# Kernel optimization log

Hardware: AMD Instinct MI355X
Metric: run time of the kernel (lower is better)

## Reference

```python
import jax, jax.numpy as jnp
import numpy as np

N_HEADS = 16
SEG_LEN = 512
MSG_LEN = 1536
T_TOTAL = SEG_LEN + MSG_LEN  # 2048


def _build_mask(T):
    # rows < SEG_LEN: attend to all cols < SEG_LEN (full, non-causal block)
    # rows >= SEG_LEN: standard causal (cols <= row)
    rows = jnp.arange(T)[:, None]
    cols = jnp.arange(T)[None, :]
    mask = jnp.where(rows < SEG_LEN, cols < SEG_LEN, cols <= rows)
    return mask  # [T, T] bool


def setup_inputs() -> dict:
    key = jax.random.key(0)
    k1, k2, k3 = jax.random.split(key, 3)
    B, T, E = 4, T_TOTAL, 1024
    x = jax.random.normal(k1, (B, T, E), dtype=jnp.float32)
    W_qkv = jax.random.normal(k2, (E, 3 * E), dtype=jnp.float32) * (1.0 / np.sqrt(E))
    b_qkv = jnp.zeros((3 * E,), dtype=jnp.float32)
    W_proj = jax.random.normal(k3, (E, E), dtype=jnp.float32) * (1.0 / np.sqrt(E))
    b_proj = jnp.zeros((E,), dtype=jnp.float32)
    return {"x": x, "W_qkv": W_qkv, "b_qkv": b_qkv, "W_proj": W_proj, "b_proj": b_proj}


def reference(x, W_qkv, b_qkv, W_proj, b_proj):
    B, T, E = x.shape
    H = N_HEADS
    D = E // H
    qkv = x @ W_qkv + b_qkv  # [B, T, 3E]
    q, k, v = jnp.split(qkv, 3, axis=-1)
    # [B, H, T, D]
    q = q.reshape(B, T, H, D).transpose(0, 2, 1, 3)
    k = k.reshape(B, T, H, D).transpose(0, 2, 1, 3)
    v = v.reshape(B, T, H, D).transpose(0, 2, 1, 3)
    att = jnp.einsum("bhqd,bhkd->bhqk", q, k) * (1.0 / np.sqrt(D))
    mask = _build_mask(T)  # [T, T]
    att = jnp.where(mask[None, None], att, jnp.float32(-jnp.inf))
    att = jax.nn.softmax(att, axis=-1)
    y = jnp.einsum("bhqk,bhkd->bhqd", att, v)
    y = y.transpose(0, 2, 1, 3).reshape(B, T, E)
    return y @ W_proj + b_proj
```

## Files before the change

### kernel.cpp

```cpp
#include <hip/hip_runtime.h>


typedef _Float16 f16;
typedef _Float16 f16x4 __attribute__((ext_vector_type(4)));
typedef _Float16 f16x8 __attribute__((ext_vector_type(8)));
typedef float f32x4 __attribute__((ext_vector_type(4)));

#define MFMA16x32(a, b, c) __builtin_amdgcn_mfma_f32_16x16x32_f16(a, b, c, 0, 0, 0)
#define MFMA16x16(a, b, c) __builtin_amdgcn_mfma_f32_16x16x16f16(a, b, c, 0, 0, 0)

__device__ __forceinline__ void gload_lds16(const void* g, void* l) {
  __builtin_amdgcn_global_load_lds(
      (__attribute__((address_space(1))) void*)g,
      (__attribute__((address_space(3))) void*)l, 16, 0, 0);
}


__global__ __launch_bounds__(256) void k_prep(
    const float* __restrict__ x, f16* __restrict__ xh,
    const float* __restrict__ Wq, f16* __restrict__ Wqt,
    const float* __restrict__ Wp, f16* __restrict__ Wpt) {
  __shared__ float tile[32][33];
  const int bid = blockIdx.x;
  if (bid < 8192) {
    int i = bid * 256 + threadIdx.x;
    float4 v = ((const float4*)x)[i];
    f16x4 o = {(f16)v.x, (f16)v.y, (f16)v.z, (f16)v.w};
    ((f16x4*)xh)[i] = o;
    return;
  }
  const float* W;
  f16* Wt;
  int Ndim, bx, by;
  if (bid < 8192 + 3072) {
    int r = bid - 8192;
    W = Wq; Wt = Wqt; Ndim = 3072; bx = r % 96; by = r / 96;
  } else {
    int r = bid - 11264;
    W = Wp; Wt = Wpt; Ndim = 1024; bx = r % 32; by = r / 32;
  }
  const int tx = threadIdx.x & 31, ty = threadIdx.x >> 5;
  const int n = bx * 32 + tx;
  const int k0 = by * 32;
  for (int j = ty; j < 32; j += 8)
    tile[j][tx] = W[(size_t)(k0 + j) * Ndim + n];
  __syncthreads();
  const int k = k0 + tx;
  for (int j = ty; j < 32; j += 8)
    Wt[(size_t)(bx * 32 + j) * 1024 + k] = (f16)tile[tx][j];
}


__global__ __launch_bounds__(256) void k_gemm_qkv(
    const f16* __restrict__ A, const f16* __restrict__ Bt,
    const float* __restrict__ bias,
    f16* __restrict__ Qo, f16* __restrict__ Ko, f16* __restrict__ Vo) {
  constexpr int KD = 1024;
  __shared__ __align__(16) f16 smem[2 * 128 * 64];
  f16* As = smem;
  f16* Bs = smem + 128 * 64;
  const int tid = threadIdx.x;
  const int wave = tid >> 6, lane = tid & 63;
  const int g = lane >> 4, l16 = lane & 15;
  const int m0 = blockIdx.y * 128, n0 = blockIdx.x * 128;
  const int wm = (wave >> 1) * 64, wn = (wave & 1) * 64;
  const int srow = wave * 8 + (lane >> 3);
  const int skc = ((lane & 7) ^ (lane >> 3)) * 8;

  f32x4 acc[4][4] = {};

  for (int k0 = 0; k0 < KD; k0 += 64) {
    __syncthreads();
    for (int it = 0; it < 4; ++it) {
      gload_lds16(A + (size_t)(m0 + it * 32 + srow) * KD + k0 + skc,
                  As + (it * 32 + wave * 8) * 64);
      gload_lds16(Bt + (size_t)(n0 + it * 32 + srow) * KD + k0 + skc,
                  Bs + (it * 32 + wave * 8) * 64);
    }
    __syncthreads();
    for (int kk = 0; kk < 64; kk += 32) {
      const int ks = kk >> 3;
      f16x8 af[4], bf[4];
      for (int mi = 0; mi < 4; ++mi) {
        int R = wm + mi * 16 + l16, sw = R & 7;
        af[mi] = *(const f16x8*)(As + R * 64 + ((ks + g) ^ sw) * 8);
      }
      for (int ni = 0; ni < 4; ++ni) {
        int R = wn + ni * 16 + l16, sw = R & 7;
        bf[ni] = *(const f16x8*)(Bs + R * 64 + ((ks + g) ^ sw) * 8);
      }
      for (int mi = 0; mi < 4; ++mi)
        for (int ni = 0; ni < 4; ++ni)
          acc[mi][ni] = MFMA16x32(af[mi], bf[ni], acc[mi][ni]);
    }
  }

  const int nsub = n0 + wn;
  const int part = nsub >> 10;
  const int h    = (nsub >> 6) & 15;
  const int mg   = m0 + wm;
  const int b    = mg >> 11;
  const int tb   = mg & 2047;
  const size_t bh = (size_t)(b * 16 + h);

  float bv[4];
  for (int ni = 0; ni < 4; ++ni) bv[ni] = bias[nsub + ni * 16 + l16];

  __syncthreads();
  f16* Es = smem + wave * 4096;

  for (int mi = 0; mi < 4; ++mi)
    for (int ni = 0; ni < 4; ++ni)
      for (int r = 0; r < 4; ++r) {
        f16 hv = (f16)(acc[mi][ni][r] + bv[ni]);
        int mrow = mi * 16 + g * 4 + r, ncol = ni * 16 + l16;
        if (part == 2)
          Es[ncol * 64 + (mrow ^ ((ncol & 7) << 3))] = hv;
        else
          Es[mrow * 64 + (ncol ^ ((mrow & 7) << 3))] = hv;
      }

  const int rrow = lane >> 3, rj = lane & 7;
  for (int p = 0; p < 8; ++p) {
    int row = p * 8 + rrow;
    f16x8 vv = *(const f16x8*)(Es + row * 64 + (rj ^ (row & 7)) * 8);
    int rcol = rj * 8;
    if (part == 0)
      *(f16x8*)(Qo + (bh * 2048 + tb + row) * 64 + rcol) = vv;
    else if (part == 1)
      *(f16x8*)(Ko + (bh * 2048 + tb + row) * 64 + rcol) = vv;
    else
      *(f16x8*)(Vo + (bh * 64 + row) * 2048 + tb + rcol) = vv;
  }
}


__global__ __launch_bounds__(256, 4) void k_attn(
    const f16* __restrict__ Q, const f16* __restrict__ Kb,
    const f16* __restrict__ Vt, f16* __restrict__ Y) {
  __shared__ __align__(16) f16 Ks[2][64 * 64];
  __shared__ __align__(16) f16 Vs[2][64 * 64];
  __shared__ float rs[4 * 32];

  const int tid = threadIdx.x;
  const int wave = tid >> 6, lane = tid & 63;
  const int g = lane >> 4, l16 = lane & 15;
  const int bh = blockIdx.x;
  const int b = bh >> 4, h = bh & 15;
  const int qt = 15 - blockIdx.y;
  const int q0 = qt * 128;
  const int nt = (qt < 4) ? 8 : (qt + 1) * 2;
  const int srowrel = lane >> 3;
  const int sc = (lane & 7) ^ srowrel;

  const f32x4 sinit = {-8.65617025f, -8.65617025f, -8.65617025f, -8.65617025f};

  f16x8 aq[2][2];
  for (int mi = 0; mi < 2; ++mi) {
    const f16* qrow =
        Q + ((size_t)bh * 2048 + q0 + wave * 32 + mi * 16 + l16) * 64 + g * 8;
    aq[mi][0] = *(const f16x8*)(qrow);
    aq[mi][1] = *(const f16x8*)(qrow + 32);
    for (int kb = 0; kb < 2; ++kb)
      aq[mi][kb] = aq[mi][kb] * (f16)0.18033688f;
  }

  f32x4 o[2][4] = {};
  float rsum[2] = {};

  for (int it = 0; it < 2; ++it) {
    int row = it * 32 + wave * 8 + srowrel;
    gload_lds16(Kb + ((size_t)bh * 2048 + row) * 64 + sc * 8,
                &Ks[0][(it * 32 + wave * 8) * 64]);
    gload_lds16(Vt + ((size_t)bh * 64 + row) * 2048 + sc * 8,
                &Vs[0][(it * 32 + wave * 8) * 64]);
  }
  __syncthreads();

  int cur = 0;
  for (int i = 0; i < nt; ++i) {
    if (i + 1 < nt) {
      const int kn0 = (i + 1) << 6;
      for (int it = 0; it < 2; ++it) {
        int row = it * 32 + wave * 8 + srowrel;
        gload_lds16(Kb + ((size_t)bh * 2048 + kn0 + row) * 64 + sc * 8,
                    &Ks[cur ^ 1][(it * 32 + wave * 8) * 64]);
        gload_lds16(Vt + ((size_t)bh * 64 + row) * 2048 + kn0 + sc * 8,
                    &Vs[cur ^ 1][(it * 32 + wave * 8) * 64]);
      }
    }

    const int kt0 = i << 6;
    const f16* Kc = Ks[cur];
    const f16* Vc = Vs[cur];

    f32x4 t[2][4];
    for (int nb = 0; nb < 4; ++nb) {
      int R = nb * 16 + l16, sw = R & 7;
      f16x8 bk0 = *(const f16x8*)(Kc + R * 64 + ((0 + g) ^ sw) * 8);
      f16x8 bk1 = *(const f16x8*)(Kc + R * 64 + ((4 + g) ^ sw) * 8);
      for (int mi = 0; mi < 2; ++mi) {
        f32x4 acc = MFMA16x32(bk0, aq[mi][0], sinit);
        t[mi][nb] = MFMA16x32(bk1, aq[mi][1], acc);
      }
    }

    const bool masked = (q0 >= 512) && (kt0 >= q0);
    f16x4 ap[4][2];
    for (int mi = 0; mi < 2; ++mi) {
      const int mrow = q0 + wave * 32 + mi * 16 + l16;
      for (int nb = 0; nb < 4; ++nb)
        for (int r = 0; r < 4; ++r) {
          float pv = __builtin_amdgcn_exp2f(t[mi][nb][r]);
          if (masked && (kt0 + nb * 16 + g * 4 + r > mrow)) pv = 0.f;
          rsum[mi] += pv;
          ap[nb][mi][r] = (f16)pv;
        }
    }

    for (int db = 0; db < 4; ++db)
      for (int nb = 0; nb < 4; ++nb) {
        int R = db * 16 + l16, sw = R & 7;
        int c = nb * 2 + (g >> 1);
        f16x4 bv = *(const f16x4*)(Vc + R * 64 + (c ^ sw) * 8 + (g & 1) * 4);
        for (int mi = 0; mi < 2; ++mi)
          o[mi][db] = MFMA16x16(ap[nb][mi], bv, o[mi][db]);
      }

    __syncthreads();
    cur ^= 1;
  }

  for (int mi = 0; mi < 2; ++mi) {
    rsum[mi] += __shfl_xor(rsum[mi], 16, 64);
    rsum[mi] += __shfl_xor(rsum[mi], 32, 64);
  }

  if (g == 0)
    for (int mi = 0; mi < 2; ++mi) rs[wave * 32 + mi * 16 + l16] = rsum[mi];
  float rinv[2][4];
  for (int mi = 0; mi < 2; ++mi)
    for (int r = 0; r < 4; ++r)
      rinv[mi][r] = 1.0f / rs[wave * 32 + mi * 16 + g * 4 + r];

  const size_t ybase = (size_t)b * 2048 + q0 + wave * 32;
  for (int mi = 0; mi < 2; ++mi)
    for (int db = 0; db < 4; ++db)
      for (int r = 0; r < 4; ++r)
        Y[(ybase + mi * 16 + g * 4 + r) * 1024 + h * 64 + db * 16 + l16] =
            (f16)(o[mi][db][r] * rinv[mi][r]);
}


__global__ __launch_bounds__(256) void k_gemm_proj(
    const f16* __restrict__ A, const f16* __restrict__ Bt,
    const float* __restrict__ bias, float* __restrict__ out) {
  constexpr int KD = 1024;
  __shared__ __align__(16) f16 As[128 * 64];
  __shared__ __align__(16) f16 Bs[128 * 64];
  const int tid = threadIdx.x;
  const int wave = tid >> 6, lane = tid & 63;
  const int g = lane >> 4, l16 = lane & 15;
  const int m0 = blockIdx.y * 128, n0 = blockIdx.x * 128;
  const int wm = (wave >> 1) * 64, wn = (wave & 1) * 64;
  const int srow = wave * 8 + (lane >> 3);
  const int skc = ((lane & 7) ^ (lane >> 3)) * 8;

  f32x4 acc[4][4] = {};

  for (int k0 = 0; k0 < KD; k0 += 64) {
    __syncthreads();
    for (int it = 0; it < 4; ++it) {
      gload_lds16(A + (size_t)(m0 + it * 32 + srow) * KD + k0 + skc,
                  As + (it * 32 + wave * 8) * 64);
      gload_lds16(Bt + (size_t)(n0 + it * 32 + srow) * KD + k0 + skc,
                  Bs + (it * 32 + wave * 8) * 64);
    }
    __syncthreads();
    for (int kk = 0; kk < 64; kk += 32) {
      const int ks = kk >> 3;
      f16x8 af[4], bf[4];
      for (int mi = 0; mi < 4; ++mi) {
        int R = wm + mi * 16 + l16, sw = R & 7;
        af[mi] = *(const f16x8*)(As + R * 64 + ((ks + g) ^ sw) * 8);
      }
      for (int ni = 0; ni < 4; ++ni) {
        int R = wn + ni * 16 + l16, sw = R & 7;
        bf[ni] = *(const f16x8*)(Bs + R * 64 + ((ks + g) ^ sw) * 8);
      }
      for (int mi = 0; mi < 4; ++mi)
        for (int ni = 0; ni < 4; ++ni)
          acc[mi][ni] = MFMA16x32(af[mi], bf[ni], acc[mi][ni]);
    }
  }

  float bv[4];
  for (int ni = 0; ni < 4; ++ni) bv[ni] = bias[n0 + wn + ni * 16 + l16];

  for (int mi = 0; mi < 4; ++mi)
    for (int ni = 0; ni < 4; ++ni)
      for (int r = 0; r < 4; ++r) {
        int m = m0 + wm + mi * 16 + g * 4 + r;
        int n = n0 + wn + ni * 16 + l16;
        out[(size_t)m * 1024 + n] = acc[mi][ni][r] + bv[ni];
      }
}


extern "C" void kernel_launch(void* const* d_in, const int* in_sizes, int n_in,
                              void* d_out, int out_size, void* d_ws,
                              size_t ws_size, hipStream_t stream) {
  const float* x      = (const float*)d_in[0];
  const float* W_qkv  = (const float*)d_in[1];
  const float* b_qkv  = (const float*)d_in[2];
  const float* W_proj = (const float*)d_in[3];
  const float* b_proj = (const float*)d_in[4];
  float* out = (float*)d_out;

  char* ws = (char*)d_ws;
  f16* xh    = (f16*)ws;   ws += (size_t)8192 * 1024 * 2;
  f16* Wqt   = (f16*)ws;   ws += (size_t)3072 * 1024 * 2;
  f16* Wpt   = (f16*)ws;   ws += (size_t)1024 * 1024 * 2;
  f16* Qb    = (f16*)ws;   ws += (size_t)64 * 2048 * 64 * 2;
  f16* Kb    = (f16*)ws;   ws += (size_t)64 * 2048 * 64 * 2;
  f16* Vt    = (f16*)ws;   ws += (size_t)64 * 64 * 2048 * 2;
  f16* Y = xh;

  k_prep<<<12288, 256, 0, stream>>>(x, xh, W_qkv, Wqt, W_proj, Wpt);
  k_gemm_qkv<<<dim3(24, 64), 256, 0, stream>>>(xh, Wqt, b_qkv, Qb, Kb, Vt);
  k_attn<<<dim3(64, 16), 256, 0, stream>>>(Qb, Kb, Vt, Y);
  k_gemm_proj<<<dim3(8, 64), 256, 0, stream>>>(Y, Wpt, b_proj, out);
}
```

Before: 263.4 us.

## Enlarge attention query tile to 256 rows and skip fully masked sub-tiles

Each attention block now handles 256 query rows (64 per wave) instead of 128, so every K/V tile loaded into LDS is reused across twice as many queries, halving K/V traffic and the number of blocks. Within the causal region, 16-row query sub-tiles that lie entirely above the diagonal for the current key tile skip their QK and PV MFMAs. The cost is a much larger register footprint (occupancy hint lowered from 4 to 2) and fewer, longer blocks (512 total), which may hurt load balance and latency hiding. Blocks are ordered so the heaviest causal tiles are launched first.

```diff
diff --git a/kernel.cpp b/kernel.cpp
--- a/kernel.cpp
+++ b/kernel.cpp
@@ -135,38 +135,41 @@
 }
 
 
-__global__ __launch_bounds__(256, 4) void k_attn(
+__global__ __launch_bounds__(256, 2) void k_attn(
     const f16* __restrict__ Q, const f16* __restrict__ Kb,
     const f16* __restrict__ Vt, f16* __restrict__ Y) {
   __shared__ __align__(16) f16 Ks[2][64 * 64];
   __shared__ __align__(16) f16 Vs[2][64 * 64];
-  __shared__ float rs[4 * 32];
+  __shared__ float rs[4 * 64];
 
   const int tid = threadIdx.x;
   const int wave = tid >> 6, lane = tid & 63;
   const int g = lane >> 4, l16 = lane & 15;
   const int bh = blockIdx.x;
   const int b = bh >> 4, h = bh & 15;
-  const int qt = 15 - blockIdx.y;
-  const int q0 = qt * 128;
-  const int nt = (qt < 4) ? 8 : (qt + 1) * 2;
+  const int by = blockIdx.y;
+  const int qb = (by < 4) ? (7 - by) : (by - 4);
+  const int q0 = qb * 256;
+  const int nt = (qb < 2) ? 8 : 4 * (qb + 1);
+  const int qw = q0 + wave * 64;
+  const bool causal = (q0 >= 512);
   const int srowrel = lane >> 3;
   const int sc = (lane & 7) ^ srowrel;
 
   const f32x4 sinit = {-8.65617025f, -8.65617025f, -8.65617025f, -8.65617025f};
 
-  f16x8 aq[2][2];
-  for (int mi = 0; mi < 2; ++mi) {
+  f16x8 aq[4][2];
+  for (int mi = 0; mi < 4; ++mi) {
     const f16* qrow =
-        Q + ((size_t)bh * 2048 + q0 + wave * 32 + mi * 16 + l16) * 64 + g * 8;
+        Q + ((size_t)bh * 2048 + qw + mi * 16 + l16) * 64 + g * 8;
     aq[mi][0] = *(const f16x8*)(qrow);
     aq[mi][1] = *(const f16x8*)(qrow + 32);
     for (int kb = 0; kb < 2; ++kb)
       aq[mi][kb] = aq[mi][kb] * (f16)0.18033688f;
   }
 
-  f32x4 o[2][4] = {};
-  float rsum[2] = {};
+  f32x4 o[4][4] = {};
+  float rsum[4] = {};
 
   for (int it = 0; it < 2; ++it) {
     int row = it * 32 + wave * 8 + srowrel;
@@ -194,27 +197,34 @@
     const f16* Kc = Ks[cur];
     const f16* Vc = Vs[cur];
 
-    f32x4 t[2][4];
+    bool act[4];
+    for (int mi = 0; mi < 4; ++mi)
+      act[mi] = !causal || (kt0 <= qw + mi * 16 + 15);
+
+    f16x8 bk0[4], bk1[4];
     for (int nb = 0; nb < 4; ++nb) {
       int R = nb * 16 + l16, sw = R & 7;
-      f16x8 bk0 = *(const f16x8*)(Kc + R * 64 + ((0 + g) ^ sw) * 8);
-      f16x8 bk1 = *(const f16x8*)(Kc + R * 64 + ((4 + g) ^ sw) * 8);
-      for (int mi = 0; mi < 2; ++mi) {
-        f32x4 acc = MFMA16x32(bk0, aq[mi][0], sinit);
-        t[mi][nb] = MFMA16x32(bk1, aq[mi][1], acc);
-      }
-    }
-
-    const bool masked = (q0 >= 512) && (kt0 >= q0);
-    f16x4 ap[4][2];
-    for (int mi = 0; mi < 2; ++mi) {
-      const int mrow = q0 + wave * 32 + mi * 16 + l16;
+      bk0[nb] = *(const f16x8*)(Kc + R * 64 + ((0 + g) ^ sw) * 8);
+      bk1[nb] = *(const f16x8*)(Kc + R * 64 + ((4 + g) ^ sw) * 8);
+    }
+
+    f16x4 ap[4][4];
+    for (int mi = 0; mi < 4; ++mi) {
+      if (!act[mi]) continue;
+      f32x4 t[4];
+      for (int nb = 0; nb < 4; ++nb) {
+        f32x4 acc = MFMA16x32(bk0[nb], aq[mi][0], sinit);
+        t[nb] = MFMA16x32(bk1[nb], aq[mi][1], acc);
+      }
+      const int mbase = qw + mi * 16;
+      const bool masked = causal && (kt0 + 63 > mbase);
+      const int mrow = mbase + l16;
       for (int nb = 0; nb < 4; ++nb)
         for (int r = 0; r < 4; ++r) {
-          float pv = __builtin_amdgcn_exp2f(t[mi][nb][r]);
+          float pv = __builtin_amdgcn_exp2f(t[nb][r]);
           if (masked && (kt0 + nb * 16 + g * 4 + r > mrow)) pv = 0.f;
           rsum[mi] += pv;
-          ap[nb][mi][r] = (f16)pv;
+          ap[mi][nb][r] = (f16)pv;
         }
     }
 
@@ -223,28 +233,28 @@
         int R = db * 16 + l16, sw = R & 7;
         int c = nb * 2 + (g >> 1);
         f16x4 bv = *(const f16x4*)(Vc + R * 64 + (c ^ sw) * 8 + (g & 1) * 4);
-        for (int mi = 0; mi < 2; ++mi)
-          o[mi][db] = MFMA16x16(ap[nb][mi], bv, o[mi][db]);
+        for (int mi = 0; mi < 4; ++mi)
+          if (act[mi]) o[mi][db] = MFMA16x16(ap[mi][nb], bv, o[mi][db]);
       }
 
     __syncthreads();
     cur ^= 1;
   }
 
-  for (int mi = 0; mi < 2; ++mi) {
+  for (int mi = 0; mi < 4; ++mi) {
     rsum[mi] += __shfl_xor(rsum[mi], 16, 64);
     rsum[mi] += __shfl_xor(rsum[mi], 32, 64);
   }
 
   if (g == 0)
-    for (int mi = 0; mi < 2; ++mi) rs[wave * 32 + mi * 16 + l16] = rsum[mi];
-  float rinv[2][4];
-  for (int mi = 0; mi < 2; ++mi)
+    for (int mi = 0; mi < 4; ++mi) rs[wave * 64 + mi * 16 + l16] = rsum[mi];
+  float rinv[4][4];
+  for (int mi = 0; mi < 4; ++mi)
     for (int r = 0; r < 4; ++r)
-      rinv[mi][r] = 1.0f / rs[wave * 32 + mi * 16 + g * 4 + r];
-
-  const size_t ybase = (size_t)b * 2048 + q0 + wave * 32;
-  for (int mi = 0; mi < 2; ++mi)
+      rinv[mi][r] = 1.0f / rs[wave * 64 + mi * 16 + g * 4 + r];
+
+  const size_t ybase = (size_t)b * 2048 + qw;
+  for (int mi = 0; mi < 4; ++mi)
     for (int db = 0; db < 4; ++db)
       for (int r = 0; r < 4; ++r)
         Y[(ybase + mi * 16 + g * 4 + r) * 1024 + h * 64 + db * 16 + l16] =
@@ -328,6 +338,6 @@
 
   k_prep<<<12288, 256, 0, stream>>>(x, xh, W_qkv, Wqt, W_proj, Wpt);
   k_gemm_qkv<<<dim3(24, 64), 256, 0, stream>>>(xh, Wqt, b_qkv, Qb, Kb, Vt);
-  k_attn<<<dim3(64, 16), 256, 0, stream>>>(Qb, Kb, Vt, Y);
+  k_attn<<<dim3(64, 8), 256, 0, stream>>>(Qb, Kb, Vt, Y);
   k_gemm_proj<<<dim3(8, 64), 256, 0, stream>>>(Y, Wpt, b_proj, out);
 }
```

Result: slower. 286.4 us (+8.7%).
